# Performance work log

Hardware: AMD Instinct MI355X
Metric: run time of the kernel (lower is better)

## Reference

```python
import math
import jax, jax.numpy as jnp
import numpy as np

T = 4096
D_MODEL = 1024
NUM_HEADS = 16
HEAD_DIM = D_MODEL // NUM_HEADS


def setup_inputs() -> dict:
    key = jax.random.key(0)
    k_x, k_wqkv, k_wproj = jax.random.split(key, 3)
    # match eqx.nn.Linear init scale: U(-1/sqrt(in), 1/sqrt(in)); randn*small works too,
    # but keep magnitudes reasonable so softmax isn't saturated.
    s_in = 1.0 / math.sqrt(D_MODEL)
    x = jax.random.normal(k_x, (T, D_MODEL), dtype=jnp.float32)
    W_qkv = jax.random.normal(k_wqkv, (3 * D_MODEL, D_MODEL), dtype=jnp.float32) * s_in
    b_qkv = jnp.zeros((3 * D_MODEL,), dtype=jnp.float32)
    W_proj = jax.random.normal(k_wproj, (D_MODEL, D_MODEL), dtype=jnp.float32) * s_in
    b_proj = jnp.zeros((D_MODEL,), dtype=jnp.float32)
    return {"x": x, "W_qkv": W_qkv, "b_qkv": b_qkv, "W_proj": W_proj, "b_proj": b_proj}


def reference(x, W_qkv, b_qkv, W_proj, b_proj):
    T_, C = x.shape  # (seq, d_model)
    H, hd = NUM_HEADS, HEAD_DIM
    # c_attn: eqx Linear computes W @ x + b per token -> x @ W.T + b
    qkv = x @ W_qkv.T + b_qkv  # (T, 3C)
    q, k, v = jnp.split(qkv, 3, axis=1)
    # (T, C) -> (H, T, hd)
    q = q.reshape(T_, H, hd).swapaxes(0, 1)
    k = k.reshape(T_, H, hd).swapaxes(0, 1)
    v = v.reshape(T_, H, hd).swapaxes(0, 1)
    scores = jnp.einsum("htd,hsd->hts", q, k) / math.sqrt(hd)  # (H, T, T)
    causal = jnp.tril(jnp.ones((T_, T_), dtype=bool))
    scores = jnp.where(causal, scores, -jnp.inf)
    attn = jax.nn.softmax(scores, axis=-1)
    y = jnp.einsum("hts,hsd->htd", attn, v)  # (H, T, hd)
    y = y.swapaxes(0, 1).reshape(T_, C)
    y = y @ W_proj.T + b_proj
    return y
```

## Files before the change

### kernel.cpp

```cpp
#include <hip/hip_runtime.h>
#include <math.h>
#include <string.h>

#define T_SEQ 4096
#define DM 1024
#define NH 16
#define HD 64

typedef short s8v __attribute__((ext_vector_type(8)));
typedef float f4v __attribute__((ext_vector_type(4)));

__device__ inline unsigned short f2bf(float f) {
    unsigned u; memcpy(&u, &f, 4);
    u = u + 0x7fffu + ((u >> 16) & 1u);
    return (unsigned short)(u >> 16);
}

__device__ inline float bf2f(unsigned short s) {
    unsigned u = (unsigned)s << 16;
    float f; memcpy(&f, &u, 4);
    return f;
}

__device__ inline float exp2fn(float x) {
#if __has_builtin(__builtin_amdgcn_exp2f)
    return __builtin_amdgcn_exp2f(x);
#else
    return exp2f(x);
#endif
}

__device__ inline void gld_lds16(const void* g, void* l) {
    __builtin_amdgcn_global_load_lds(
        (const __attribute__((address_space(1))) void*)g,
        (__attribute__((address_space(3))) void*)l, 16, 0, 0);
}

__global__ __launch_bounds__(256)
void cvt3(const float* __restrict__ i0, unsigned short* __restrict__ o0, int n0,
          const float* __restrict__ i1, unsigned short* __restrict__ o1, int n1,
          const float* __restrict__ i2, unsigned short* __restrict__ o2, int n2) {
    int i = blockIdx.x * 256 + threadIdx.x;
    const float* in; unsigned short* out; int j;
    if (i < n0)           { in = i0; out = o0; j = i; }
    else if (i < n0 + n1) { in = i1; out = o1; j = i - n0; }
    else if (i < n0 + n1 + n2) { in = i2; out = o2; j = i - n0 - n1; }
    else return;
    const float4* p = (const float4*)(in + (size_t)j * 8);
    float4 a = p[0], b = p[1];
    unsigned short o[8] = {f2bf(a.x), f2bf(a.y), f2bf(a.z), f2bf(a.w),
                           f2bf(b.x), f2bf(b.y), f2bf(b.z), f2bf(b.w)};
    uint4 pk; memcpy(&pk, o, 16);
    *(uint4*)(out + (size_t)j * 8) = pk;
}

__global__ __launch_bounds__(256)
void binit(const float* __restrict__ bias, float* __restrict__ out) {
    int i = blockIdx.x * 256 + threadIdx.x;
    int col4 = (i & (DM / 4 - 1)) * 4;
    float4 b = *(const float4*)&bias[col4];
    *(float4*)&out[(size_t)i * 4] = b;
}

template<int MODE, int TN, int OCC>
__global__ __launch_bounds__(256, OCC)
void gemm_bt_mfma(const unsigned short* __restrict__ A, const unsigned short* __restrict__ B,
                  const float* __restrict__ bias, void* __restrict__ Cout,
                  unsigned short* __restrict__ qbuf, unsigned short* __restrict__ kbuf2,
                  unsigned short* __restrict__ vT,
                  int M, int N, int K, int nbx, int patchw, int patchh, int kspl) {
    constexpr int NF = TN / 32;
    __shared__ __align__(16) short As[2][4096];
    __shared__ __align__(16) short Bs[2][TN * 32];
    const int tid = threadIdx.x;
    const int w = tid >> 6, lane = tid & 63;
    const int wr = w >> 1, wc = w & 1;

    const int bpk = 8 * patchw * patchh;
    const int s = blockIdx.x / bpk;
    const int bl = blockIdx.x % bpk;
    const int ks = s * (K / kspl), ke = ks + K / kspl;
    const int xcd = bl & 7, ii = bl >> 3;
    const int pxn = nbx / patchw;
    const int bx = (xcd % pxn) * patchw + ii % patchw;
    const int by = (xcd / pxn) * patchh + ii / patchw;
    const int m0 = by * 128, n0 = bx * TN;

    const bool doA = (w < 2);
    const bool doStage = doA || ((w & 1) * 64 < TN);
    const unsigned short* src = doA ? A : B;
    const int rbase = (doA ? m0 : n0) + (w & 1) * 64;
    const unsigned short* gsrc = src + (size_t)(rbase + (lane & 15)) * K + ((lane >> 4) * 8);
    const int ldoff = ((w & 1) * 4) * 512;

    f4v acc[4][NF];
    #pragma unroll
    for (int i = 0; i < 4; ++i)
        #pragma unroll
        for (int j = 0; j < NF; ++j) acc[i][j] = (f4v){0.f, 0.f, 0.f, 0.f};

    auto stage = [&](short* base, int k0) {
        short* ldst = base + ldoff;
        #pragma unroll
        for (int i = 0; i < 4; ++i)
            gld_lds16(gsrc + (size_t)(i * 16) * K + k0, ldst + i * 512);
    };
    auto compute = [&](const short* Ab, const short* Bb) {
        s8v af[4], bfr[NF];
        #pragma unroll
        for (int i = 0; i < 4; ++i) af[i] = *(const s8v*)&Ab[((wr * 4 + i) * 64 + lane) * 8];
        #pragma unroll
        for (int j = 0; j < NF; ++j) bfr[j] = *(const s8v*)&Bs[0][0];
        #pragma unroll
        for (int j = 0; j < NF; ++j) bfr[j] = *(const s8v*)&Bb[((wc * NF + j) * 64 + lane) * 8];
        #pragma unroll
        for (int i = 0; i < 4; ++i)
            #pragma unroll
            for (int j = 0; j < NF; ++j)
                acc[i][j] = __builtin_amdgcn_mfma_f32_16x16x32_bf16(af[i], bfr[j], acc[i][j], 0, 0, 0);
    };

    if (doStage) stage(doA ? As[0] : Bs[0], ks);
    __syncthreads();
    for (int k0 = ks; k0 < ke; k0 += 64) {
        if (doStage) stage(doA ? As[1] : Bs[1], k0 + 32);
        compute(As[0], Bs[0]);
        __syncthreads();
        if (doStage && (k0 + 64 < ke)) stage(doA ? As[0] : Bs[0], k0 + 64);
        compute(As[1], Bs[1]);
        __syncthreads();
    }

    const int l15 = lane & 15, quad = lane >> 4;

    if (MODE == 2 && n0 >= 2 * DM) {
        float bj[NF];
        #pragma unroll
        for (int j = 0; j < NF; ++j) bj[j] = bias[n0 + wc * (TN / 2) + j * 16 + l15];
        const int tile = (m0 + wr * 64) >> 6;
        const int hh = ((n0 - 2 * DM) >> 6) + (TN == 128 ? wc : 0);
        #pragma unroll
        for (int i = 0; i < 4; ++i) {
            #pragma unroll
            for (int j = 0; j < NF; ++j) {
                const int ob = (TN == 128) ? j : (wc * 2 + j);
                unsigned short o[4];
                #pragma unroll
                for (int rg = 0; rg < 4; ++rg) o[rg] = f2bf(acc[i][j][rg] + bj[j]);
                unsigned long long pk; memcpy(&pk, o, 8);
                size_t off = (size_t)hh * 262144 + (size_t)tile * 4096
                           + (size_t)((ob * 2 + (i >> 1)) * 64 + lane) * 8 + (i & 1) * 4;
                *(unsigned long long*)&vT[off] = pk;
            }
        }
    } else if (MODE == 2) {
        float bj[NF];
        #pragma unroll
        for (int j = 0; j < NF; ++j) bj[j] = bias[n0 + wc * (TN / 2) + j * 16 + l15];
        unsigned short* dst = (n0 < DM) ? qbuf : kbuf2;
        const int nb = (n0 < DM) ? n0 : n0 - DM;
        #pragma unroll
        for (int i = 0; i < 4; ++i) {
            #pragma unroll
            for (int rg = 0; rg < 4; ++rg) {
                int row = m0 + wr * 64 + i * 16 + quad * 4 + rg;
                #pragma unroll
                for (int j = 0; j < NF; ++j) {
                    int col = nb + wc * (TN / 2) + j * 16 + l15;
                    dst[(size_t)row * DM + col] = f2bf(acc[i][j][rg] + bj[j]);
                }
            }
        }
    } else if (MODE == 3) {
        float* outp = (float*)Cout;
        #pragma unroll
        for (int i = 0; i < 4; ++i) {
            #pragma unroll
            for (int rg = 0; rg < 4; ++rg) {
                int row = m0 + wr * 64 + i * 16 + quad * 4 + rg;
                #pragma unroll
                for (int j = 0; j < NF; ++j) {
                    int col = n0 + wc * (TN / 2) + j * 16 + l15;
                    unsafeAtomicAdd(&outp[(size_t)row * N + col], acc[i][j][rg]);
                }
            }
        }
    } else {
        float bj[NF];
        #pragma unroll
        for (int j = 0; j < NF; ++j) bj[j] = bias[n0 + wc * (TN / 2) + j * 16 + l15];
        #pragma unroll
        for (int i = 0; i < 4; ++i) {
            #pragma unroll
            for (int rg = 0; rg < 4; ++rg) {
                int row = m0 + wr * 64 + i * 16 + quad * 4 + rg;
                #pragma unroll
                for (int j = 0; j < NF; ++j) {
                    int col = n0 + wc * (TN / 2) + j * 16 + l15;
                    ((float*)Cout)[(size_t)row * N + col] = acc[i][j][rg] + bj[j];
                }
            }
        }
    }
}

__device__ __forceinline__ void soft_step(f4v* st, bool diag, int qloc, int quad,
                                          float& lr, s8v& pf0, s8v& pf1) {
    const float C2  = 0.1803368851f;
    const float MC2 = 12.0f * 0.1803368851f;
    float sv[4][4];
    #pragma unroll
    for (int kb = 0; kb < 4; ++kb)
        #pragma unroll
        for (int rg = 0; rg < 4; ++rg) {
            float s = st[kb][rg];
            if (diag && (kb * 16 + quad * 4 + rg > qloc)) s = -3.0e38f;
            float t = exp2fn(fmaf(s, C2, -MC2));
            sv[kb][rg] = t;
            lr += t;
        }
    int pk[4][2];
    #pragma unroll
    for (int kb = 0; kb < 4; ++kb) {
        unsigned u0 = __float_as_uint(sv[kb][0]) + 0x8000u;
        unsigned u1 = __float_as_uint(sv[kb][1]) + 0x8000u;
        unsigned u2 = __float_as_uint(sv[kb][2]) + 0x8000u;
        unsigned u3 = __float_as_uint(sv[kb][3]) + 0x8000u;
        pk[kb][0] = (int)__builtin_amdgcn_perm(u1, u0, 0x07060302);
        pk[kb][1] = (int)__builtin_amdgcn_perm(u3, u2, 0x07060302);
    }
    int4 a = {pk[0][0], pk[0][1], pk[1][0], pk[1][1]};
    int4 b = {pk[2][0], pk[2][1], pk[3][0], pk[3][1]};
    memcpy(&pf0, &a, 16);
    memcpy(&pf1, &b, 16);
}

__global__ __launch_bounds__(256, 3)
void attn_mfma7(const unsigned short* __restrict__ qb,
                const unsigned short* __restrict__ kbf,
                const unsigned short* __restrict__ vT,
                unsigned short* __restrict__ y0,
                unsigned short* __restrict__ y1,
                unsigned short* __restrict__ y2,
                float* __restrict__ lsum) {
    const int b = blockIdx.x;
    const int par = b % 3;
    const int idx = b / 3;
    const int h = idx & 15, a = idx >> 4;
    const int tid = threadIdx.x;
    const int w = tid >> 6, lane = tid & 63;
    const int quad = lane >> 4, l15 = lane & 15;
    const int cq = h * HD;
    unsigned short* ypar = (par == 0) ? y0 : (par == 1) ? y1 : y2;
    float* lpar = lsum + ((size_t)par * NH + h) * T_SEQ;
    const unsigned short* vbase = vT + (size_t)h * 262144;

    __shared__ short KB[2][4096];
    __shared__ short VTs[2][4096];
    __shared__ short QB[8192];

    for (int ph = 0; ph < 2; ++ph) {
        const int qt = ph ? (31 - a) : a;
        const int q0 = qt * 128;
        const int kmax = 2 * qt + 1;
        const int nk = (kmax >= par) ? (kmax - par) / 3 + 1 : 0;
        const int kt0 = par * 64;

        __syncthreads();
        #pragma unroll
        for (int rr = 0; rr < 4; ++rr) {
            int ch = rr * 256 + tid;
            int qg = ch >> 7, hf = (ch >> 6) & 1, ln = ch & 63;
            gld_lds16(qb + (size_t)(q0 + qg * 16 + (ln & 15)) * DM + cq + hf * 32 + ((ln >> 4) << 3),
                      &QB[(ch & ~63) * 8]);
        }
        if (nk > 0) {
            #pragma unroll
            for (int rr = 0; rr < 2; ++rr) {
                int ch = rr * 256 + tid;
                int blk = ch >> 7, hf = (ch >> 6) & 1, ln = ch & 63;
                gld_lds16(kbf + (size_t)(kt0 + blk * 16 + (ln & 15)) * DM + cq + hf * 32 + ((ln >> 4) << 3),
                          &KB[0][(ch & ~63) * 8]);
                gld_lds16(vbase + (size_t)(kt0 >> 6) * 4096 + (size_t)ch * 8,
                          &VTs[0][(ch & ~63) * 8]);
            }
        }
        __syncthreads();

        s8v qf[2][2];
        #pragma unroll
        for (int g = 0; g < 2; ++g)
            #pragma unroll
            for (int hf = 0; hf < 2; ++hf)
                qf[g][hf] = *(const s8v*)&QB[((((g * 4 + w) * 2 + hf) * 64) + lane) * 8];

        f4v O0[4], O1[4];
        #pragma unroll
        for (int ob = 0; ob < 4; ++ob) {
            O0[ob] = (f4v){0.f, 0.f, 0.f, 0.f};
            O1[ob] = (f4v){0.f, 0.f, 0.f, 0.f};
        }
        float lr0 = 0.f, lr1 = 0.f;

        for (int i = 0; i < nk; ++i) {
            const int kt = par + 3 * i;
            const int p = i & 1;
            const bool g0a = (kt <= 2 * qt);
            const bool m0 = (kt == 2 * qt);
            const bool m1 = (kt == 2 * qt + 1);
            if (i < nk - 1) {
                const int k1 = kt0 + (i + 1) * 192;
                #pragma unroll
                for (int rr = 0; rr < 2; ++rr) {
                    int ch = rr * 256 + tid;
                    int blk = ch >> 7, hf = (ch >> 6) & 1, ln = ch & 63;
                    gld_lds16(kbf + (size_t)(k1 + blk * 16 + (ln & 15)) * DM + cq
                                  + hf * 32 + ((ln >> 4) << 3),
                              &KB[p ^ 1][(ch & ~63) * 8]);
                    gld_lds16(vbase + (size_t)(k1 >> 6) * 4096 + (size_t)ch * 8,
                              &VTs[p ^ 1][(ch & ~63) * 8]);
                }
            }

            f4v st0[4], st1[4];
            #pragma unroll
            for (int kb = 0; kb < 4; ++kb) {
                s8v k0f = *(const s8v*)&KB[p][((kb * 2 + 0) * 64 + lane) * 8];
                s8v k1f = *(const s8v*)&KB[p][((kb * 2 + 1) * 64 + lane) * 8];
                f4v c1 = (f4v){0.f, 0.f, 0.f, 0.f};
                c1 = __builtin_amdgcn_mfma_f32_16x16x32_bf16(k0f, qf[1][0], c1, 0, 0, 0);
                c1 = __builtin_amdgcn_mfma_f32_16x16x32_bf16(k1f, qf[1][1], c1, 0, 0, 0);
                st1[kb] = c1;
                if (g0a) {
                    f4v c0 = (f4v){0.f, 0.f, 0.f, 0.f};
                    c0 = __builtin_amdgcn_mfma_f32_16x16x32_bf16(k0f, qf[0][0], c0, 0, 0, 0);
                    c0 = __builtin_amdgcn_mfma_f32_16x16x32_bf16(k1f, qf[0][1], c0, 0, 0, 0);
                    st0[kb] = c0;
                }
            }

            s8v pf10, pf11, pf00, pf01;
            soft_step(st1, m1, w * 16 + l15, quad, lr1, pf10, pf11);
            if (g0a) soft_step(st0, m0, w * 16 + l15, quad, lr0, pf00, pf01);

            #pragma unroll
            for (int ob = 0; ob < 4; ++ob) {
                s8v v0f = *(const s8v*)&VTs[p][((ob * 2 + 0) * 64 + lane) * 8];
                s8v v1f = *(const s8v*)&VTs[p][((ob * 2 + 1) * 64 + lane) * 8];
                O1[ob] = __builtin_amdgcn_mfma_f32_16x16x32_bf16(v0f, pf10, O1[ob], 0, 0, 0);
                O1[ob] = __builtin_amdgcn_mfma_f32_16x16x32_bf16(v1f, pf11, O1[ob], 0, 0, 0);
                if (g0a) {
                    O0[ob] = __builtin_amdgcn_mfma_f32_16x16x32_bf16(v0f, pf00, O0[ob], 0, 0, 0);
                    O0[ob] = __builtin_amdgcn_mfma_f32_16x16x32_bf16(v1f, pf01, O0[ob], 0, 0, 0);
                }
            }
            __syncthreads();
        }

        lr0 += __shfl_xor(lr0, 16); lr0 += __shfl_xor(lr0, 32);
        lr1 += __shfl_xor(lr1, 16); lr1 += __shfl_xor(lr1, 32);
        #pragma unroll
        for (int g = 0; g < 2; ++g) {
            const f4v* O = g ? O1 : O0;
            int qrow = q0 + g * 64 + w * 16 + l15;
            size_t ybase = (size_t)qrow * DM + cq;
            #pragma unroll
            for (int ob = 0; ob < 4; ++ob) {
                unsigned short o[4];
                #pragma unroll
                for (int rg = 0; rg < 4; ++rg) o[rg] = f2bf(O[ob][rg]);
                unsigned long long pk; memcpy(&pk, o, 8);
                *(unsigned long long*)&ypar[ybase + ob * 16 + quad * 4] = pk;
            }
            if (quad == 0) lpar[qrow] = g ? lr1 : lr0;
        }
    }
}

__global__ __launch_bounds__(256)
void attn_combine3(const unsigned short* __restrict__ y0,
                   const unsigned short* __restrict__ y1,
                   const unsigned short* __restrict__ y2,
                   const float* __restrict__ lsum,
                   unsigned short* __restrict__ yout) {
    int i = blockIdx.x * 256 + threadIdx.x;
    int t = i >> 7, d8 = i & 127;
    int h = d8 >> 3;
    float l = lsum[(size_t)h * T_SEQ + t]
            + lsum[((size_t)NH + h) * T_SEQ + t]
            + lsum[((size_t)2 * NH + h) * T_SEQ + t];
    float inv = 1.f / l;
    size_t off = (size_t)t * DM + d8 * 8;
    uint4 ua = *(const uint4*)(y0 + off);
    uint4 ub = *(const uint4*)(y1 + off);
    uint4 uc = *(const uint4*)(y2 + off);
    const unsigned short* pa = (const unsigned short*)&ua;
    const unsigned short* pb = (const unsigned short*)&ub;
    const unsigned short* pc = (const unsigned short*)&uc;
    unsigned short o[8];
    #pragma unroll
    for (int k = 0; k < 8; ++k)
        o[k] = f2bf((bf2f(pa[k]) + bf2f(pb[k]) + bf2f(pc[k])) * inv);
    uint4 pk; memcpy(&pk, o, 16);
    *(uint4*)(yout + off) = pk;
}

extern "C" void kernel_launch(void* const* d_in, const int* in_sizes, int n_in,
                              void* d_out, int out_size, void* d_ws, size_t ws_size,
                              hipStream_t stream) {
    const float* x     = (const float*)d_in[0];
    const float* Wqkv  = (const float*)d_in[1];
    const float* bqkv  = (const float*)d_in[2];
    const float* Wproj = (const float*)d_in[3];
    const float* bproj = (const float*)d_in[4];
    float* out = (float*)d_out;

    char* ws = (char*)d_ws;
    unsigned short* qbuf  = (unsigned short*)(ws);
    unsigned short* kbuf  = (unsigned short*)(ws + ( 8u << 20));
    unsigned short* vTb   = (unsigned short*)(ws + (16u << 20));
    unsigned short* yattb = (unsigned short*)(ws + (24u << 20));
    float*          lsum  = (float*)         (ws + (34u << 20));
    unsigned short* xb    = (unsigned short*)(ws + (35u << 20));
    unsigned short* wqkvb = (unsigned short*)(ws + (43u << 20));
    unsigned short* wprjb = (unsigned short*)(ws + (32u << 20));
    unsigned short* y0p   = (unsigned short*)(ws + (35u << 20));
    unsigned short* y1p   = (unsigned short*)(ws + (43u << 20));
    unsigned short* y2p   = (unsigned short*)(ws + (51u << 20));

    dim3 blk(256);
    {
        int n0 = T_SEQ * DM / 8, n1 = 3 * DM * DM / 8, n2 = DM * DM / 8;
        cvt3<<<dim3((n0 + n1 + n2 + 255) / 256), blk, 0, stream>>>(
            x, xb, n0, Wqkv, wqkvb, n1, Wproj, wprjb, n2);
    }
    binit<<<dim3(T_SEQ * DM / 4 / 256), blk, 0, stream>>>(bproj, out);
    gemm_bt_mfma<2, 64, 6><<<dim3(1536), blk, 0, stream>>>(
        xb, wqkvb, bqkv, nullptr, qbuf, kbuf, vTb, T_SEQ, 3 * DM, DM, 48, 24, 8, 1);
    attn_mfma7<<<dim3(768), blk, 0, stream>>>(qbuf, kbuf, vTb, y0p, y1p, y2p, lsum);
    attn_combine3<<<dim3(T_SEQ * DM / 8 / 256), blk, 0, stream>>>(y0p, y1p, y2p, lsum, yattb);
    gemm_bt_mfma<3, 64, 4><<<dim3(1024), blk, 0, stream>>>(
        yattb, wprjb, bproj, out, nullptr, nullptr, nullptr, T_SEQ, DM, DM, 16, 8, 8, 2);
}
```

Before: 260.8 us.

## Triple-buffer GEMM LDS pipeline with one barrier per step and widen QKV tile

```diff
diff --git a/kernel.cpp b/kernel.cpp
--- a/kernel.cpp
+++ b/kernel.cpp
@@ -70,16 +70,16 @@
                   unsigned short* __restrict__ vT,
                   int M, int N, int K, int nbx, int patchw, int patchh, int kspl) {
     constexpr int NF = TN / 32;
-    __shared__ __align__(16) short As[2][4096];
-    __shared__ __align__(16) short Bs[2][TN * 32];
+    __shared__ __align__(16) short As[3][4096];
+    __shared__ __align__(16) short Bs[3][TN * 32];
     const int tid = threadIdx.x;
     const int w = tid >> 6, lane = tid & 63;
     const int wr = w >> 1, wc = w & 1;
 
     const int bpk = 8 * patchw * patchh;
-    const int s = blockIdx.x / bpk;
+    const int s0 = blockIdx.x / bpk;
     const int bl = blockIdx.x % bpk;
-    const int ks = s * (K / kspl), ke = ks + K / kspl;
+    const int ks = s0 * (K / kspl), ke = ks + K / kspl;
     const int xcd = bl & 7, ii = bl >> 3;
     const int pxn = nbx / patchw;
     const int bx = (xcd % pxn) * patchw + ii % patchw;
@@ -99,8 +99,8 @@
         #pragma unroll
         for (int j = 0; j < NF; ++j) acc[i][j] = (f4v){0.f, 0.f, 0.f, 0.f};
 
-    auto stage = [&](short* base, int k0) {
-        short* ldst = base + ldoff;
+    auto stage = [&](int buf, int k0) {
+        short* ldst = (doA ? As[buf] : Bs[buf]) + ldoff;
         #pragma unroll
         for (int i = 0; i < 4; ++i)
             gld_lds16(gsrc + (size_t)(i * 16) * K + k0, ldst + i * 512);
@@ -110,8 +110,6 @@
         #pragma unroll
         for (int i = 0; i < 4; ++i) af[i] = *(const s8v*)&Ab[((wr * 4 + i) * 64 + lane) * 8];
         #pragma unroll
-        for (int j = 0; j < NF; ++j) bfr[j] = *(const s8v*)&Bs[0][0];
-        #pragma unroll
         for (int j = 0; j < NF; ++j) bfr[j] = *(const s8v*)&Bb[((wc * NF + j) * 64 + lane) * 8];
         #pragma unroll
         for (int i = 0; i < 4; ++i)
@@ -120,15 +118,19 @@
                 acc[i][j] = __builtin_amdgcn_mfma_f32_16x16x32_bf16(af[i], bfr[j], acc[i][j], 0, 0, 0);
     };
 
-    if (doStage) stage(doA ? As[0] : Bs[0], ks);
-    __syncthreads();
-    for (int k0 = ks; k0 < ke; k0 += 64) {
-        if (doStage) stage(doA ? As[1] : Bs[1], k0 + 32);
-        compute(As[0], Bs[0]);
-        __syncthreads();
-        if (doStage && (k0 + 64 < ke)) stage(doA ? As[0] : Bs[0], k0 + 64);
-        compute(As[1], Bs[1]);
-        __syncthreads();
+    const int nstep = (ke - ks) >> 5;
+    if (doStage) stage(0, ks);
+    for (int s = 0; s < nstep; ++s) {
+        if (s + 1 < nstep) {
+            if (doStage) stage((s + 1) % 3, ks + (s + 1) * 32);
+            asm volatile("s_waitcnt vmcnt(4)" ::: "memory");
+        } else {
+            asm volatile("s_waitcnt vmcnt(0)" ::: "memory");
+        }
+        __builtin_amdgcn_s_barrier();
+        asm volatile("" ::: "memory");
+        const int cb = s % 3;
+        compute(As[cb], Bs[cb]);
     }
 
     const int l15 = lane & 15, quad = lane >> 4;
@@ -420,10 +422,10 @@
     unsigned short* kbuf  = (unsigned short*)(ws + ( 8u << 20));
     unsigned short* vTb   = (unsigned short*)(ws + (16u << 20));
     unsigned short* yattb = (unsigned short*)(ws + (24u << 20));
+    unsigned short* wprjb = (unsigned short*)(ws + (32u << 20));
     float*          lsum  = (float*)         (ws + (34u << 20));
     unsigned short* xb    = (unsigned short*)(ws + (35u << 20));
     unsigned short* wqkvb = (unsigned short*)(ws + (43u << 20));
-    unsigned short* wprjb = (unsigned short*)(ws + (32u << 20));
     unsigned short* y0p   = (unsigned short*)(ws + (35u << 20));
     unsigned short* y1p   = (unsigned short*)(ws + (43u << 20));
     unsigned short* y2p   = (unsigned short*)(ws + (51u << 20));
@@ -435,8 +437,8 @@
             x, xb, n0, Wqkv, wqkvb, n1, Wproj, wprjb, n2);
     }
     binit<<<dim3(T_SEQ * DM / 4 / 256), blk, 0, stream>>>(bproj, out);
-    gemm_bt_mfma<2, 64, 6><<<dim3(1536), blk, 0, stream>>>(
-        xb, wqkvb, bqkv, nullptr, qbuf, kbuf, vTb, T_SEQ, 3 * DM, DM, 48, 24, 8, 1);
+    gemm_bt_mfma<2, 128, 3><<<dim3(768), blk, 0, stream>>>(
+        xb, wqkvb, bqkv, nullptr, qbuf, kbuf, vTb, T_SEQ, 3 * DM, DM, 24, 6, 16, 1);
     attn_mfma7<<<dim3(768), blk, 0, stream>>>(qbuf, kbuf, vTb, y0p, y1p, y2p, lsum);
     attn_combine3<<<dim3(T_SEQ * DM / 8 / 256), blk, 0, stream>>>(y0p, y1p, y2p, lsum, yattb);
     gemm_bt_mfma<3, 64, 4><<<dim3(1024), blk, 0, stream>>>(
```

Result: faster. 237.8 us (-8.8%).
